# Optimization experiments

Hardware: AMD Instinct MI355X
Metric: run time of the kernel (lower is better)

The kernel has to match this reference:

```python
import jax, jax.numpy as jnp
import numpy as np

N_NODES = 8192
N_EDGES = 32768
D = 768
H1 = 8
NEG_SLOPE = 0.2


def setup_inputs() -> dict:
    key = jax.random.key(0)
    ks = jax.random.split(key, 10)
    s = 0.02  # init scale keeps attention logits numerically tame
    x = jax.random.normal(ks[0], (N_NODES, D), dtype=jnp.float32)
    edge_index = jax.random.randint(ks[1], (2, N_EDGES), 0, N_NODES, dtype=jnp.int64)
    W1 = jax.random.normal(ks[2], (D, H1 * D), dtype=jnp.float32) * s
    a_src1 = jax.random.normal(ks[3], (H1, D), dtype=jnp.float32) * s
    a_dst1 = jax.random.normal(ks[4], (H1, D), dtype=jnp.float32) * s
    b1 = jnp.zeros((H1 * D,), dtype=jnp.float32)
    W2 = jax.random.normal(ks[5], (H1 * D, D), dtype=jnp.float32) * s
    a_src2 = jax.random.normal(ks[6], (1, D), dtype=jnp.float32) * s
    a_dst2 = jax.random.normal(ks[7], (1, D), dtype=jnp.float32) * s
    b2 = jnp.zeros((D,), dtype=jnp.float32)
    return {"x": x, "edge_index": edge_index, "W1": W1, "a_src1": a_src1,
            "a_dst1": a_dst1, "b1": b1, "W2": W2, "a_src2": a_src2,
            "a_dst2": a_dst2, "b2": b2}


def gat_conv(x, src, dst, W, a_src, a_dst, b, heads, out_ch):
    """PyG GATConv (concat=True, self-loops already appended to src/dst)."""
    n = x.shape[0]
    h = (x @ W).reshape(n, heads, out_ch)            # [N,H,C]
    alpha_src = jnp.einsum("nhc,hc->nh", h, a_src)  # [N,H]
    alpha_dst = jnp.einsum("nhc,hc->nh", h, a_dst)  # [N,H]
    # edge scores: leaky_relu(a_src.h_j + a_dst.h_i) for edge j->i
    e = jax.nn.leaky_relu(alpha_src[src] + alpha_dst[dst], NEG_SLOPE)  # [E,H]
    # segment softmax over incoming edges of each destination node
    m = jax.ops.segment_max(e, dst, num_segments=n)   # [N,H]
    m = jnp.where(jnp.isfinite(m), m, 0.0)
    p = jnp.exp(e - m[dst])                           # [E,H]
    denom = jax.ops.segment_sum(p, dst, num_segments=n)
    alpha = p / denom[dst]                            # [E,H]
    msg = h[src] * alpha[:, :, None]                  # [E,H,C] gather+weight
    out = jax.ops.segment_sum(msg, dst, num_segments=n)  # [N,H,C] scatter-add
    return out.reshape(n, heads * out_ch) + b


def reference(x, edge_index, W1, a_src1, a_dst1, b1, W2, a_src2, a_dst2, b2):
    n = x.shape[0]
    loops = jnp.arange(n, dtype=edge_index.dtype)
    src = jnp.concatenate([edge_index[0], loops])  # add_self_loops=True
    dst = jnp.concatenate([edge_index[1], loops])
    h = gat_conv(x, src, dst, W1, a_src1, a_dst1, b1, H1, D)
    h = jax.nn.elu(h)
    out = gat_conv(h, src, dst, W2, a_src2, a_dst2, b2, 1, D)
    return out
```

## Files before the change

kernel.cpp:

```cpp
#include <hip/hip_runtime.h>
#include <hip/hip_bf16.h>


#define N_NODES 8192
#define N_EDGES 32768
#define E_TOT   (N_EDGES + N_NODES)
#define D_IN    768
#define H1      8
#define HC1     (H1 * D_IN)
#define KSPLIT  4
#define KSLICE  (HC1 / KSPLIT)

typedef unsigned short ushort_t;
using short8  = __attribute__((ext_vector_type(8))) short;
using floatx4 = __attribute__((ext_vector_type(4))) float;

__device__ __forceinline__ float bf2f(unsigned short u) {
  return __uint_as_float(((unsigned)u) << 16);
}
__device__ __forceinline__ unsigned short f2bf(float f) {
  unsigned u = __float_as_uint(f);
  unsigned r = (u + 0x7fffu + ((u >> 16) & 1u)) >> 16;
  return (unsigned short)r;
}

__global__ __launch_bounds__(64) void frag_transpose_kernel(
    const float* __restrict__ W, ushort_t* __restrict__ out,
    int Kdim, int Ndim) {
  const int bn = blockIdx.x;
  const int bk = blockIdx.y;
  const int lane = threadIdx.x;
  const int lrow = lane & 15, lq = lane >> 4;
  const int n = bn * 16 + lrow;
  const int kb = bk * 32 + lq * 8;
  ushort_t v[8];
#pragma unroll
  for (int e = 0; e < 8; ++e)
    v[e] = f2bf(W[(size_t)(kb + e) * Ndim + n]);
  *(short8*)(out + ((size_t)bn * (Kdim >> 5) + bk) * 512 + lane * 8) =
      *(short8*)v;
}

__global__ void prep_aw_kernel(const float* __restrict__ W1,
                               const float* __restrict__ aS,
                               const float* __restrict__ aD,
                               float* __restrict__ awS,
                               float* __restrict__ awD) {
  const int d = blockIdx.x;
  const int t = threadIdx.x;
  const float* row = W1 + (size_t)d * HC1;
  float ps[H1], pd[H1];
#pragma unroll
  for (int h = 0; h < H1; ++h) { ps[h] = 0.f; pd[h] = 0.f; }
#pragma unroll
  for (int h = 0; h < H1; ++h)
#pragma unroll
    for (int j = 0; j < 3; ++j) {
      int idx = h * 768 + j * 256 + t;
      float w = row[idx];
      ps[h] += w * aS[idx];
      pd[h] += w * aD[idx];
    }
#pragma unroll
  for (int h = 0; h < H1; ++h)
    for (int off = 32; off > 0; off >>= 1) {
      ps[h] += __shfl_down(ps[h], off, 64);
      pd[h] += __shfl_down(pd[h], off, 64);
    }
  __shared__ float red[2][4][H1];
  int w = t >> 6;
  if ((t & 63) == 0) {
#pragma unroll
    for (int h = 0; h < H1; ++h) { red[0][w][h] = ps[h]; red[1][w][h] = pd[h]; }
  }
  __syncthreads();
  if (t < H1)
    awS[d * H1 + t] = red[0][0][t] + red[0][1][t] + red[0][2][t] + red[0][3][t];
  else if (t >= 64 && t < 64 + H1) {
    int h = t - 64;
    awD[d * H1 + h] = red[1][0][h] + red[1][1][h] + red[1][2][h] + red[1][3][h];
  }
}

__global__ void node_prep_kernel(const float* __restrict__ x,
                                 const float* __restrict__ awS,
                                 const float* __restrict__ awD,
                                 ushort_t* __restrict__ xb,
                                 float* __restrict__ as1,
                                 float* __restrict__ ad1) {
  const int n = blockIdx.x;
  const int t = threadIdx.x;
  float ps[H1], pd[H1];
#pragma unroll
  for (int h = 0; h < H1; ++h) { ps[h] = 0.f; pd[h] = 0.f; }
#pragma unroll
  for (int j = 0; j < 3; ++j) {
    int d = j * 256 + t;
    float xv = x[(size_t)n * 768 + d];
    xb[(size_t)n * 768 + d] = f2bf(xv);
    const float4* s4 = (const float4*)(awS + d * 8);
    const float4* d4 = (const float4*)(awD + d * 8);
    float4 a0 = s4[0], a1 = s4[1];
    float4 c0 = d4[0], c1 = d4[1];
    ps[0] += xv * a0.x; ps[1] += xv * a0.y; ps[2] += xv * a0.z; ps[3] += xv * a0.w;
    ps[4] += xv * a1.x; ps[5] += xv * a1.y; ps[6] += xv * a1.z; ps[7] += xv * a1.w;
    pd[0] += xv * c0.x; pd[1] += xv * c0.y; pd[2] += xv * c0.z; pd[3] += xv * c0.w;
    pd[4] += xv * c1.x; pd[5] += xv * c1.y; pd[6] += xv * c1.z; pd[7] += xv * c1.w;
  }
#pragma unroll
  for (int h = 0; h < H1; ++h)
    for (int off = 32; off > 0; off >>= 1) {
      ps[h] += __shfl_down(ps[h], off, 64);
      pd[h] += __shfl_down(pd[h], off, 64);
    }
  __shared__ float red[2][4][H1];
  int w = t >> 6;
  if ((t & 63) == 0) {
#pragma unroll
    for (int h = 0; h < H1; ++h) { red[0][w][h] = ps[h]; red[1][w][h] = pd[h]; }
  }
  __syncthreads();
  if (t < H1)
    as1[n * H1 + t] = red[0][0][t] + red[0][1][t] + red[0][2][t] + red[0][3][t];
  else if (t >= 64 && t < 64 + H1) {
    int h = t - 64;
    ad1[n * H1 + h] = red[1][0][h] + red[1][1][h] + red[1][2][h] + red[1][3][h];
  }
}

__global__ void deg_kernel(const int* __restrict__ dst, int* __restrict__ deg) {
  int e = blockIdx.x * blockDim.x + threadIdx.x;
  if (e >= E_TOT) return;
  int d = (e < N_EDGES) ? dst[e] : (e - N_EDGES);
  atomicAdd(&deg[d], 1);
}

__global__ void scan_kernel(const int* __restrict__ deg, int* __restrict__ start,
                            int* __restrict__ cursor) {
  __shared__ int sums[1024];
  int t = threadIdx.x;
  int base = t * 8;
  int local[8];
  int s = 0;
#pragma unroll
  for (int i = 0; i < 8; ++i) { local[i] = s; s += deg[base + i]; }
  sums[t] = s;
  __syncthreads();
  for (int off = 1; off < 1024; off <<= 1) {
    int v = (t >= off) ? sums[t - off] : 0;
    __syncthreads();
    sums[t] += v;
    __syncthreads();
  }
  int excl = (t == 0) ? 0 : sums[t - 1];
#pragma unroll
  for (int i = 0; i < 8; ++i) {
    int st = excl + local[i];
    start[base + i] = st;
    cursor[base + i] = st;
  }
}

__global__ void fill_kernel(const int* __restrict__ dst, int* __restrict__ cursor,
                            int* __restrict__ csr) {
  int e = blockIdx.x * blockDim.x + threadIdx.x;
  if (e >= E_TOT) return;
  int d = (e < N_EDGES) ? dst[e] : (e - N_EDGES);
  int pos = atomicAdd(&cursor[d], 1);
  csr[pos] = e;
}

__global__ __launch_bounds__(256) void attn1_kernel(
    const ushort_t* __restrict__ xb, const float* __restrict__ as1,
    const float* __restrict__ ad1, const int* __restrict__ start,
    const int* __restrict__ deg, const int* __restrict__ csr,
    const int* __restrict__ src, ushort_t* __restrict__ z_sw) {
  const int n = blockIdx.x;
  const int t = threadIdx.x;
  const int st = start[n], dg = deg[n];
  const int h = t & 7, eloc = t >> 3;
  __shared__ float invd[H1];
  __shared__ float alphaS[32][H1];
  __shared__ int sidx[32];
  __shared__ float red[4][H1];

  const float adv = ad1[n * H1 + h];
  float pden = 0.f;
  for (int base = 0; base < dg; base += 32) {
    int ei = base + eloc;
    if (ei < dg) {
      int e = csr[st + ei];
      int s = (e < N_EDGES) ? src[e] : (e - N_EDGES);
      float l = as1[s * H1 + h] + adv;
      l = l > 0.f ? l : 0.2f * l;
      pden += __expf(l);
    }
  }
  pden += __shfl_down(pden, 8, 64);
  pden += __shfl_down(pden, 16, 64);
  pden += __shfl_down(pden, 32, 64);
  if ((t & 63) < 8) red[t >> 6][h] = pden;
  __syncthreads();
  if (t < 8) invd[t] = 1.0f / (red[0][t] + red[1][t] + red[2][t] + red[3][t]);
  __syncthreads();

  int hp[3], ip[3];
#pragma unroll
  for (int p = 0; p < 3; ++p) {
    int c8 = p * 256 + t;
    hp[p] = c8 / 96;
    ip[p] = c8 % 96;
  }
  float acc[3][8];
#pragma unroll
  for (int p = 0; p < 3; ++p)
#pragma unroll
    for (int e = 0; e < 8; ++e) acc[p][e] = 0.f;

  for (int base = 0; base < dg; base += 32) {
    int cnt = dg - base; if (cnt > 32) cnt = 32;
    if (eloc < cnt) {
      int e = csr[st + base + eloc];
      int s = (e < N_EDGES) ? src[e] : (e - N_EDGES);
      float l = as1[s * H1 + h] + adv;
      l = l > 0.f ? l : 0.2f * l;
      alphaS[eloc][h] = __expf(l) * invd[h];
      if (h == 0) sidx[eloc] = s;
    }
    __syncthreads();
    for (int ei = 0; ei < cnt; ++ei) {
      int s = sidx[ei];
      const uint4* xrow = (const uint4*)(xb + (size_t)s * 768);
#pragma unroll
      for (int p = 0; p < 3; ++p) {
        uint4 v = xrow[ip[p]];
        float al = alphaS[ei][hp[p]];
        unsigned uu[4] = {v.x, v.y, v.z, v.w};
#pragma unroll
        for (int q = 0; q < 4; ++q) {
          acc[p][2 * q]     += al * __uint_as_float(uu[q] << 16);
          acc[p][2 * q + 1] += al * __uint_as_float(uu[q] & 0xffff0000u);
        }
      }
    }
    __syncthreads();
  }
#pragma unroll
  for (int p = 0; p < 3; ++p) {
    int c8 = p * 256 + t;
    int k = c8 * 8;
    size_t chunk = (size_t)(n >> 4) * 192 + (k >> 5);
    int word = ((k >> 3) & 3) * 16 + (n & 15);
    ushort_t v[8];
#pragma unroll
    for (int e = 0; e < 8; ++e) v[e] = f2bf(acc[p][e]);
    *(short8*)(z_sw + chunk * 512 + word * 8) = *(short8*)v;
  }
}

#define LOADI(dst, BASE, CH, kk)                                               \
  _Pragma("unroll") for (int q = 0; q < 4; ++q)                                \
      dst[q] = *(const short8*)((BASE) +                                       \
                                (((size_t)((CH)[q] + (kk))) << 9) + lane8);

#define MFMA16(af, bf)                                                         \
  _Pragma("unroll") for (int i_ = 0; i_ < 4; ++i_)                             \
      _Pragma("unroll") for (int j_ = 0; j_ < 4; ++j_)                         \
          acc[i_][j_] = __builtin_amdgcn_mfma_f32_16x16x32_bf16(               \
              af[i_], bf[j_], acc[i_][j_], 0, 0, 0);

#define GEMM_KLOOP(NCH, ABASE, BBASE)                                          \
  {                                                                            \
    short8 a0[4], b0[4], a1[4], b1[4];                                         \
    LOADI(a0, ABASE, chA, 0) LOADI(b0, BBASE, chB, 0)                          \
    LOADI(a1, ABASE, chA, 1) LOADI(b1, BBASE, chB, 1)                          \
    for (int k = 0; k < (NCH); k += 2) {                                       \
      MFMA16(a0, b0)                                                           \
      LOADI(a0, ABASE, chA, k + 2) LOADI(b0, BBASE, chB, k + 2)                \
      MFMA16(a1, b1)                                                           \
      LOADI(a1, ABASE, chA, k + 3) LOADI(b1, BBASE, chB, k + 3)                \
    }                                                                          \
  }

__global__ __launch_bounds__(256) void gemm_l1_kernel(
    const ushort_t* __restrict__ Asw, const ushort_t* __restrict__ Bsw,
    const float* __restrict__ biasb, ushort_t* __restrict__ Csw) {
  __shared__ ushort_t tile[128 * 136];
  const int id = blockIdx.x;
  const int head = id & 7;
  const int j_id = id >> 3;
  const int n_t = j_id % 6;
  const int m_t = j_id / 6;
  const int tid = threadIdx.x;
  const int lane = tid & 63;
  const int w = tid >> 6;
  const int wm = w >> 1, wn = w & 1;
  const int lrow = lane & 15, lq = lane >> 4;
  const int lane8 = lane * 8;

  int chA[4], chB[4];
#pragma unroll
  for (int q = 0; q < 4; ++q) {
    chA[q] = __builtin_amdgcn_readfirstlane((m_t * 8 + wm * 4 + q) * 192 +
                                            head * 24);
    chB[q] = __builtin_amdgcn_readfirstlane((head * 48 + n_t * 8 + wn * 4 + q) *
                                            24);
  }
  floatx4 acc[4][4];
#pragma unroll
  for (int i = 0; i < 4; ++i)
#pragma unroll
    for (int j = 0; j < 4; ++j) acc[i][j] = {0.f, 0.f, 0.f, 0.f};

  GEMM_KLOOP(24, Asw, Bsw)

  const float* bias = biasb + head * 768 + n_t * 128;
#pragma unroll
  for (int i = 0; i < 4; ++i) {
    int row_l = wm * 64 + i * 16 + lq * 4;
#pragma unroll
    for (int j = 0; j < 4; ++j) {
      int col_l = wn * 64 + j * 16 + lrow;
      float bv = bias[col_l];
#pragma unroll
      for (int r = 0; r < 4; ++r) {
        float v = acc[i][j][r] + bv;
        v = v > 0.f ? v : __expf(v) - 1.0f;
        tile[(row_l + r) * 136 + col_l] = f2bf(v);
      }
    }
  }
  __syncthreads();
#pragma unroll
  for (int cc = 0; cc < 8; ++cc) {
    int ch = w * 8 + cc;
    int RB = ch >> 2, kg = ch & 3;
    short8 vv = *(const short8*)&tile[(RB * 16 + lrow) * 136 + kg * 32 + lq * 8];
    size_t chunk_g = (size_t)(m_t * 8 + RB) * 192 + head * 24 + n_t * 4 + kg;
    *((short8*)Csw + chunk_g * 64 + lane) = vv;
  }
}

__global__ __launch_bounds__(256) void gemm_l2_kernel(
    const ushort_t* __restrict__ Asw, const ushort_t* __restrict__ Bsw,
    float* __restrict__ Cp) {
  const int id = blockIdx.x;
  const int c = id & 7;
  const int s = c >> 1;
  const int j_id = id >> 3;
  const int n_t = j_id % 6;
  const int m_t = (j_id / 6) * 2 + (c & 1);
  const int tid = threadIdx.x;
  const int lane = tid & 63;
  const int w = tid >> 6;
  const int wm = w >> 1, wn = w & 1;
  const int lrow = lane & 15, lq = lane >> 4;
  const int lane8 = lane * 8;

  int chA[4], chB[4];
#pragma unroll
  for (int q = 0; q < 4; ++q) {
    chA[q] = __builtin_amdgcn_readfirstlane((m_t * 8 + wm * 4 + q) * 192 +
                                            s * 48);
    chB[q] = __builtin_amdgcn_readfirstlane((n_t * 8 + wn * 4 + q) * 192 +
                                            s * 48);
  }
  floatx4 acc[4][4];
#pragma unroll
  for (int i = 0; i < 4; ++i)
#pragma unroll
    for (int j = 0; j < 4; ++j) acc[i][j] = {0.f, 0.f, 0.f, 0.f};

  GEMM_KLOOP(48, Asw, Bsw)

  float* C = Cp + (size_t)s * N_NODES * 768;
  const int m0 = m_t * 128, n0 = n_t * 128;
#pragma unroll
  for (int i = 0; i < 4; ++i) {
    int row_b = m0 + wm * 64 + i * 16 + lq * 4;
#pragma unroll
    for (int j = 0; j < 4; ++j) {
      int col = n0 + wn * 64 + j * 16 + lrow;
#pragma unroll
      for (int r = 0; r < 4; ++r)
        C[(size_t)(row_b + r) * 768 + col] = acc[i][j][r];
    }
  }
}

__global__ void reduce_alpha2_kernel(const float* __restrict__ parts,
                                     const float* __restrict__ aS,
                                     const float* __restrict__ aD,
                                     ushort_t* __restrict__ yb,
                                     float* __restrict__ as2,
                                     float* __restrict__ ad2) {
  const int n = blockIdx.x;
  const int t = threadIdx.x;
  const size_t S = (size_t)N_NODES * 768;
  float ps = 0.f, pd = 0.f;
#pragma unroll
  for (int j = 0; j < 3; ++j) {
    int cidx = j * 256 + t;
    size_t base = (size_t)n * 768 + cidx;
    float v = parts[base] + parts[base + S] + parts[base + 2 * S] +
              parts[base + 3 * S];
    yb[base] = f2bf(v);
    ps += v * aS[cidx];
    pd += v * aD[cidx];
  }
  for (int off = 32; off > 0; off >>= 1) {
    ps += __shfl_down(ps, off, 64);
    pd += __shfl_down(pd, off, 64);
  }
  __shared__ float red[2][4];
  int w = t >> 6;
  if ((t & 63) == 0) { red[0][w] = ps; red[1][w] = pd; }
  __syncthreads();
  if (t == 0) as2[n] = red[0][0] + red[0][1] + red[0][2] + red[0][3];
  if (t == 64) ad2[n] = red[1][0] + red[1][1] + red[1][2] + red[1][3];
}

__global__ __launch_bounds__(256) void attn2_kernel(
    const ushort_t* __restrict__ yb, const float* __restrict__ as2,
    const float* __restrict__ ad2, const int* __restrict__ start,
    const int* __restrict__ deg, const int* __restrict__ csr,
    const int* __restrict__ src, const float* __restrict__ b2,
    float* __restrict__ out) {
  const int n = blockIdx.x;
  const int t = threadIdx.x;
  const int st = start[n], dg = deg[n];
  __shared__ float alphaS[64];
  __shared__ int sidx[64];
  __shared__ float red[4];
  __shared__ float invd_sh;

  const float adv = ad2[n];
  float pden = 0.f;
  for (int ei = t; ei < dg; ei += 256) {
    int e = csr[st + ei];
    int s = (e < N_EDGES) ? src[e] : (e - N_EDGES);
    float l = as2[s] + adv;
    l = l > 0.f ? l : 0.2f * l;
    pden += __expf(l);
  }
  for (int off = 32; off > 0; off >>= 1) pden += __shfl_down(pden, off, 64);
  if ((t & 63) == 0) red[t >> 6] = pden;
  __syncthreads();
  if (t == 0) invd_sh = 1.0f / (red[0] + red[1] + red[2] + red[3]);
  __syncthreads();
  const float invd = invd_sh;

  float a0 = 0.f, a1 = 0.f, a2 = 0.f;
  for (int base = 0; base < dg; base += 64) {
    int cnt = dg - base; if (cnt > 64) cnt = 64;
    if (t < cnt) {
      int e = csr[st + base + t];
      int s = (e < N_EDGES) ? src[e] : (e - N_EDGES);
      float l = as2[s] + adv;
      l = l > 0.f ? l : 0.2f * l;
      alphaS[t] = __expf(l) * invd;
      sidx[t] = s;
    }
    __syncthreads();
    for (int ei = 0; ei < cnt; ++ei) {
      float al = alphaS[ei];
      const ushort_t* row = yb + (size_t)sidx[ei] * 768;
      a0 += al * bf2f(row[t]);
      a1 += al * bf2f(row[t + 256]);
      a2 += al * bf2f(row[t + 512]);
    }
    __syncthreads();
  }
  out[(size_t)n * 768 + t]       = a0 + b2[t];
  out[(size_t)n * 768 + t + 256] = a1 + b2[t + 256];
  out[(size_t)n * 768 + t + 512] = a2 + b2[t + 512];
}

extern "C" void kernel_launch(void* const* d_in, const int* in_sizes, int n_in,
                              void* d_out, int out_size, void* d_ws, size_t ws_size,
                              hipStream_t stream) {
  const float* x      = (const float*)d_in[0];
  const int*   ei     = (const int*)d_in[1];
  const float* W1     = (const float*)d_in[2];
  const float* a_src1 = (const float*)d_in[3];
  const float* a_dst1 = (const float*)d_in[4];
  const float* b1     = (const float*)d_in[5];
  const float* W2     = (const float*)d_in[6];
  const float* a_src2 = (const float*)d_in[7];
  const float* a_dst2 = (const float*)d_in[8];
  const float* b2     = (const float*)d_in[9];
  float* out = (float*)d_out;
  const int* src = ei;
  const int* dst = ei + N_EDGES;

  char* ws = (char*)d_ws;
  size_t off = 0;
  auto alloc = [&](size_t bytes) -> void* {
    void* p = ws + off;
    off = (off + bytes + 255) & ~(size_t)255;
    return p;
  };

  int* deg = (int*)alloc(N_NODES * 4);
  float* awS = (float*)alloc(768 * H1 * 4);
  float* awD = (float*)alloc(768 * H1 * 4);
  float* as1 = (float*)alloc(N_NODES * H1 * 4);
  float* ad1 = (float*)alloc(N_NODES * H1 * 4);
  float* as2 = (float*)alloc(N_NODES * 4);
  float* ad2 = (float*)alloc(N_NODES * 4);
  int* start  = (int*)alloc(N_NODES * 4);
  int* cursor = (int*)alloc(N_NODES * 4);
  int* csr    = (int*)alloc(E_TOT * 4);
  ushort_t* xb     = (ushort_t*)alloc((size_t)N_NODES * D_IN * 2);
  ushort_t* w1t_sw = (ushort_t*)alloc((size_t)HC1 * D_IN * 2 + 8192);
  ushort_t* w2t_sw = (ushort_t*)alloc((size_t)HC1 * D_IN * 2 + 8192);
  ushort_t* z_sw   = (ushort_t*)alloc((size_t)N_NODES * HC1 * 2 + 8192);
  ushort_t* h2b_sw = (ushort_t*)alloc((size_t)N_NODES * HC1 * 2 + 8192);
  ushort_t* yb  = xb;
  float* parts  = (float*)z_sw;
  (void)ws_size; (void)n_in; (void)in_sizes; (void)out_size;

  hipMemsetAsync(deg, 0, N_NODES * 4, stream);

  prep_aw_kernel<<<768, 256, 0, stream>>>(W1, a_src1, a_dst1, awS, awD);
  node_prep_kernel<<<N_NODES, 256, 0, stream>>>(x, awS, awD, xb, as1, ad1);
  frag_transpose_kernel<<<dim3(HC1 / 16, D_IN / 32), 64, 0, stream>>>(
      W1, w1t_sw, D_IN, HC1);
  frag_transpose_kernel<<<dim3(D_IN / 16, HC1 / 32), 64, 0, stream>>>(
      W2, w2t_sw, HC1, D_IN);

  deg_kernel<<<(E_TOT + 255) / 256, 256, 0, stream>>>(dst, deg);
  scan_kernel<<<1, 1024, 0, stream>>>(deg, start, cursor);
  fill_kernel<<<(E_TOT + 255) / 256, 256, 0, stream>>>(dst, cursor, csr);

  attn1_kernel<<<N_NODES, 256, 0, stream>>>(xb, as1, ad1, start, deg, csr,
                                            src, z_sw);
  gemm_l1_kernel<<<8 * 64 * 6, 256, 0, stream>>>(z_sw, w1t_sw, b1, h2b_sw);

  gemm_l2_kernel<<<KSPLIT * 2 * 32 * 6, 256, 0, stream>>>(h2b_sw, w2t_sw,
                                                          parts);
  reduce_alpha2_kernel<<<N_NODES, 256, 0, stream>>>(parts, a_src2, a_dst2, yb,
                                                    as2, ad2);
  attn2_kernel<<<N_NODES, 256, 0, stream>>>(yb, as2, ad2, start, deg, csr,
                                            src, b2, out);
}
```

Measured before the change: 511.6 us.

## Stage GEMM operand fragments through LDS with double-buffered global_load_lds

New measurement: 490.4 us. 1.04x faster.

```diff
diff --git a/kernel.cpp b/kernel.cpp
--- a/kernel.cpp
+++ b/kernel.cpp
@@ -22,6 +22,12 @@
   unsigned u = __float_as_uint(f);
   unsigned r = (u + 0x7fffu + ((u >> 16) & 1u)) >> 16;
   return (unsigned short)r;
+}
+
+__device__ __forceinline__ void gll16(const ushort_t* g, ushort_t* l) {
+  __builtin_amdgcn_global_load_lds(
+      (const __attribute__((address_space(1))) void*)g,
+      (__attribute__((address_space(3))) void*)l, 16, 0, 0);
 }
 
 __global__ __launch_bounds__(64) void frag_transpose_kernel(
@@ -258,34 +264,47 @@
   }
 }
 
-#define LOADI(dst, BASE, CH, kk)                                               \
-  _Pragma("unroll") for (int q = 0; q < 4; ++q)                                \
-      dst[q] = *(const short8*)((BASE) +                                       \
-                                (((size_t)((CH)[q] + (kk))) << 9) + lane8);
-
 #define MFMA16(af, bf)                                                         \
   _Pragma("unroll") for (int i_ = 0; i_ < 4; ++i_)                             \
       _Pragma("unroll") for (int j_ = 0; j_ < 4; ++j_)                         \
           acc[i_][j_] = __builtin_amdgcn_mfma_f32_16x16x32_bf16(               \
               af[i_], bf[j_], acc[i_][j_], 0, 0, 0);
 
-#define GEMM_KLOOP(NCH, ABASE, BBASE)                                          \
+#define STAGE16(b, kc)                                                         \
   {                                                                            \
-    short8 a0[4], b0[4], a1[4], b1[4];                                         \
-    LOADI(a0, ABASE, chA, 0) LOADI(b0, BBASE, chB, 0)                          \
-    LOADI(a1, ABASE, chA, 1) LOADI(b1, BBASE, chB, 1)                          \
-    for (int k = 0; k < (NCH); k += 2) {                                       \
-      MFMA16(a0, b0)                                                           \
-      LOADI(a0, ABASE, chA, k + 2) LOADI(b0, BBASE, chB, k + 2)                \
-      MFMA16(a1, b1)                                                           \
-      LOADI(a1, ABASE, chA, k + 3) LOADI(b1, BBASE, chB, k + 3)                \
+    ushort_t* ld_ = smem + (b) * 8192 + (2 * w) * 512;                         \
+    gll16(ASW + (((size_t)(cA0 + (kc))) << 9) + lane8, ld_);                   \
+    gll16(ASW + (((size_t)(cA1 + (kc))) << 9) + lane8, ld_ + 512);             \
+    gll16(BSW + (((size_t)(cB0 + (kc))) << 9) + lane8, ld_ + 4096);            \
+    gll16(BSW + (((size_t)(cB1 + (kc))) << 9) + lane8, ld_ + 4608);            \
+  }
+
+#define SBODY(b, kc, NCH)                                                      \
+  {                                                                            \
+    if ((kc) + 1 < (NCH)) STAGE16((b) ^ 1, (kc) + 1)                           \
+    const ushort_t* ra_ = smem + (b) * 8192 + wm * 2048 + lane8;               \
+    const ushort_t* rb_ = smem + (b) * 8192 + 4096 + wn * 2048 + lane8;        \
+    short8 af[4], bf[4];                                                       \
+    _Pragma("unroll") for (int q_ = 0; q_ < 4; ++q_) {                         \
+      af[q_] = *(const short8*)(ra_ + q_ * 512);                               \
+      bf[q_] = *(const short8*)(rb_ + q_ * 512);                               \
     }                                                                          \
+    MFMA16(af, bf)                                                             \
+    __syncthreads();                                                           \
+  }
+
+#define STAGED_KLOOP(NCH)                                                      \
+  STAGE16(0, 0)                                                                \
+  __syncthreads();                                                             \
+  for (int kc = 0; kc < (NCH); kc += 2) {                                      \
+    SBODY(0, kc, (NCH))                                                        \
+    SBODY(1, kc + 1, (NCH))                                                    \
   }
 
 __global__ __launch_bounds__(256) void gemm_l1_kernel(
     const ushort_t* __restrict__ Asw, const ushort_t* __restrict__ Bsw,
     const float* __restrict__ biasb, ushort_t* __restrict__ Csw) {
-  __shared__ ushort_t tile[128 * 136];
+  __shared__ ushort_t smem[17408];
   const int id = blockIdx.x;
   const int head = id & 7;
   const int j_id = id >> 3;
@@ -297,23 +316,25 @@
   const int wm = w >> 1, wn = w & 1;
   const int lrow = lane & 15, lq = lane >> 4;
   const int lane8 = lane * 8;
-
-  int chA[4], chB[4];
-#pragma unroll
-  for (int q = 0; q < 4; ++q) {
-    chA[q] = __builtin_amdgcn_readfirstlane((m_t * 8 + wm * 4 + q) * 192 +
-                                            head * 24);
-    chB[q] = __builtin_amdgcn_readfirstlane((head * 48 + n_t * 8 + wn * 4 + q) *
-                                            24);
-  }
+  const ushort_t* ASW = Asw;
+  const ushort_t* BSW = Bsw;
+
+  const int cA0 = __builtin_amdgcn_readfirstlane((m_t * 8 + 2 * w) * 192 +
+                                                 head * 24);
+  const int cA1 = cA0 + 192;
+  const int cB0 = __builtin_amdgcn_readfirstlane((head * 48 + n_t * 8 + 2 * w) *
+                                                 24);
+  const int cB1 = cB0 + 24;
+
   floatx4 acc[4][4];
 #pragma unroll
   for (int i = 0; i < 4; ++i)
 #pragma unroll
     for (int j = 0; j < 4; ++j) acc[i][j] = {0.f, 0.f, 0.f, 0.f};
 
-  GEMM_KLOOP(24, Asw, Bsw)
-
+  STAGED_KLOOP(24)
+
+  ushort_t* tile = smem;
   const float* bias = biasb + head * 768 + n_t * 128;
 #pragma unroll
   for (int i = 0; i < 4; ++i) {
@@ -344,6 +365,7 @@
 __global__ __launch_bounds__(256) void gemm_l2_kernel(
     const ushort_t* __restrict__ Asw, const ushort_t* __restrict__ Bsw,
     float* __restrict__ Cp) {
+  __shared__ ushort_t smem[16384];
   const int id = blockIdx.x;
   const int c = id & 7;
   const int s = c >> 1;
@@ -356,22 +378,23 @@
   const int wm = w >> 1, wn = w & 1;
   const int lrow = lane & 15, lq = lane >> 4;
   const int lane8 = lane * 8;
-
-  int chA[4], chB[4];
-#pragma unroll
-  for (int q = 0; q < 4; ++q) {
-    chA[q] = __builtin_amdgcn_readfirstlane((m_t * 8 + wm * 4 + q) * 192 +
-                                            s * 48);
-    chB[q] = __builtin_amdgcn_readfirstlane((n_t * 8 + wn * 4 + q) * 192 +
-                                            s * 48);
-  }
+  const ushort_t* ASW = Asw;
+  const ushort_t* BSW = Bsw;
+
+  const int cA0 = __builtin_amdgcn_readfirstlane((m_t * 8 + 2 * w) * 192 +
+                                                 s * 48);
+  const int cA1 = cA0 + 192;
+  const int cB0 = __builtin_amdgcn_readfirstlane((n_t * 8 + 2 * w) * 192 +
+                                                 s * 48);
+  const int cB1 = cB0 + 192;
+
   floatx4 acc[4][4];
 #pragma unroll
   for (int i = 0; i < 4; ++i)
 #pragma unroll
     for (int j = 0; j < 4; ++j) acc[i][j] = {0.f, 0.f, 0.f, 0.f};
 
-  GEMM_KLOOP(48, Asw, Bsw)
+  STAGED_KLOOP(48)
 
   float* C = Cp + (size_t)s * N_NODES * 768;
   const int m0 = m_t * 128, n0 = n_t * 128;
```

## Stage GEMM operands through LDS ring with async global_load_lds and larger tiles

Applied to the files above, without the earlier changes.

After: 462.4 us. 9.6% less time.

```diff
diff --git a/kernel.cpp b/kernel.cpp
--- a/kernel.cpp
+++ b/kernel.cpp
@@ -22,6 +22,12 @@
   unsigned u = __float_as_uint(f);
   unsigned r = (u + 0x7fffu + ((u >> 16) & 1u)) >> 16;
   return (unsigned short)r;
+}
+
+__device__ __forceinline__ void gll16(const ushort_t* g, ushort_t* l) {
+  __builtin_amdgcn_global_load_lds(
+      (const __attribute__((address_space(1))) void*)g,
+      (__attribute__((address_space(3))) void*)l, 16, 0, 0);
 }
 
 __global__ __launch_bounds__(64) void frag_transpose_kernel(
@@ -258,126 +264,154 @@
   }
 }
 
-#define LOADI(dst, BASE, CH, kk)                                               \
-  _Pragma("unroll") for (int q = 0; q < 4; ++q)                                \
-      dst[q] = *(const short8*)((BASE) +                                       \
-                                (((size_t)((CH)[q] + (kk))) << 9) + lane8);
-
-#define MFMA16(af, bf)                                                         \
-  _Pragma("unroll") for (int i_ = 0; i_ < 4; ++i_)                             \
-      _Pragma("unroll") for (int j_ = 0; j_ < 4; ++j_)                         \
-          acc[i_][j_] = __builtin_amdgcn_mfma_f32_16x16x32_bf16(               \
-              af[i_], bf[j_], acc[i_][j_], 0, 0, 0);
-
-#define GEMM_KLOOP(NCH, ABASE, BBASE)                                          \
+#define STAGE_RING(t)                                                          \
   {                                                                            \
-    short8 a0[4], b0[4], a1[4], b1[4];                                         \
-    LOADI(a0, ABASE, chA, 0) LOADI(b0, BBASE, chB, 0)                          \
-    LOADI(a1, ABASE, chA, 1) LOADI(b1, BBASE, chB, 1)                          \
-    for (int k = 0; k < (NCH); k += 2) {                                       \
-      MFMA16(a0, b0)                                                           \
-      LOADI(a0, ABASE, chA, k + 2) LOADI(b0, BBASE, chB, k + 2)                \
-      MFMA16(a1, b1)                                                           \
-      LOADI(a1, ABASE, chA, k + 3) LOADI(b1, BBASE, chB, k + 3)                \
-    }                                                                          \
-  }
-
-__global__ __launch_bounds__(256) void gemm_l1_kernel(
+    ushort_t* ld_ = smem + ((t) & 3) * 16384 + slot512;                        \
+    _Pragma("unroll") for (int q_ = 0; q_ < 4; ++q_)                           \
+        gll16(SRC + (((size_t)(cb[q_] + (t))) << 9) + lane8, ld_ + q_ * 512);  \
+  }
+
+#define GSTEP_BODY(s, VMSTR, NSV)                                             \
+  {                                                                           \
+    asm volatile("s_waitcnt vmcnt(" VMSTR ")" ::: "memory");                  \
+    __builtin_amdgcn_s_barrier();                                             \
+    if ((s) + 3 < (NSV)) STAGE_RING((s) + 3)                                  \
+    const ushort_t* buf_ = smem + ((s) & 3) * 16384;                          \
+    short8 af[8], bf[4];                                                      \
+    _Pragma("unroll") for (int i_ = 0; i_ < 8; ++i_)                          \
+        af[i_] = *(const short8*)(buf_ + (wm * 8 + i_) * 512 + lane8);        \
+    _Pragma("unroll") for (int j_ = 0; j_ < 4; ++j_)                          \
+        bf[j_] = *(const short8*)(buf_ + 8192 + (wn * 4 + j_) * 512 + lane8); \
+    __builtin_amdgcn_s_setprio(1);                                            \
+    _Pragma("unroll") for (int i_ = 0; i_ < 8; ++i_)                          \
+        _Pragma("unroll") for (int j_ = 0; j_ < 4; ++j_)                      \
+            acc[i_][j_] = __builtin_amdgcn_mfma_f32_16x16x32_bf16(            \
+                af[i_], bf[j_], acc[i_][j_], 0, 0, 0);                        \
+    __builtin_amdgcn_s_setprio(0);                                            \
+  }
+
+#define GEMM_PIPE(NSV)                                                        \
+  _Pragma("unroll") for (int p_ = 0; p_ < 3; ++p_) STAGE_RING(p_)             \
+  _Pragma("unroll 4") for (int s_ = 0; s_ < (NSV)-2; ++s_) {                  \
+    GSTEP_BODY(s_, "8", (NSV))                                                \
+  }                                                                           \
+  GSTEP_BODY((NSV)-2, "4", (NSV))                                             \
+  GSTEP_BODY((NSV)-1, "0", (NSV))
+
+__global__ __launch_bounds__(512, 2) void gemm_l1_kernel(
     const ushort_t* __restrict__ Asw, const ushort_t* __restrict__ Bsw,
     const float* __restrict__ biasb, ushort_t* __restrict__ Csw) {
-  __shared__ ushort_t tile[128 * 136];
+  __shared__ ushort_t smem[4 * 16384];
   const int id = blockIdx.x;
   const int head = id & 7;
   const int j_id = id >> 3;
-  const int n_t = j_id % 6;
-  const int m_t = j_id / 6;
+  const int n_t = j_id % 3;
+  const int m_t = j_id / 3;
   const int tid = threadIdx.x;
   const int lane = tid & 63;
   const int w = tid >> 6;
-  const int wm = w >> 1, wn = w & 1;
+  const int wm = w >> 2, wn = w & 3;
   const int lrow = lane & 15, lq = lane >> 4;
   const int lane8 = lane * 8;
-
-  int chA[4], chB[4];
+  const int slot512 = w * 2048;
+  const ushort_t* SRC = (w < 4) ? Asw : Bsw;
+
+  int cb[4];
 #pragma unroll
   for (int q = 0; q < 4; ++q) {
-    chA[q] = __builtin_amdgcn_readfirstlane((m_t * 8 + wm * 4 + q) * 192 +
-                                            head * 24);
-    chB[q] = __builtin_amdgcn_readfirstlane((head * 48 + n_t * 8 + wn * 4 + q) *
-                                            24);
-  }
-  floatx4 acc[4][4];
-#pragma unroll
-  for (int i = 0; i < 4; ++i)
+    int v;
+    if (w < 4)
+      v = (m_t * 16 + 4 * w + q) * 192 + head * 24;
+    else
+      v = (head * 48 + n_t * 16 + 4 * (w - 4) + q) * 24;
+    cb[q] = __builtin_amdgcn_readfirstlane(v);
+  }
+
+  floatx4 acc[8][4];
+#pragma unroll
+  for (int i = 0; i < 8; ++i)
 #pragma unroll
     for (int j = 0; j < 4; ++j) acc[i][j] = {0.f, 0.f, 0.f, 0.f};
 
-  GEMM_KLOOP(24, Asw, Bsw)
-
-  const float* bias = biasb + head * 768 + n_t * 128;
-#pragma unroll
-  for (int i = 0; i < 4; ++i) {
-    int row_l = wm * 64 + i * 16 + lq * 4;
-#pragma unroll
-    for (int j = 0; j < 4; ++j) {
-      int col_l = wn * 64 + j * 16 + lrow;
-      float bv = bias[col_l];
-#pragma unroll
-      for (int r = 0; r < 4; ++r) {
-        float v = acc[i][j][r] + bv;
-        v = v > 0.f ? v : __expf(v) - 1.0f;
-        tile[(row_l + r) * 136 + col_l] = f2bf(v);
-      }
-    }
-  }
-  __syncthreads();
-#pragma unroll
-  for (int cc = 0; cc < 8; ++cc) {
-    int ch = w * 8 + cc;
-    int RB = ch >> 2, kg = ch & 3;
-    short8 vv = *(const short8*)&tile[(RB * 16 + lrow) * 136 + kg * 32 + lq * 8];
-    size_t chunk_g = (size_t)(m_t * 8 + RB) * 192 + head * 24 + n_t * 4 + kg;
-    *((short8*)Csw + chunk_g * 64 + lane) = vv;
-  }
-}
-
-__global__ __launch_bounds__(256) void gemm_l2_kernel(
+  GEMM_PIPE(24)
+
+  ushort_t* tile = smem;
+  const float* bias = biasb + head * 768 + n_t * 256;
+#pragma unroll
+  for (int p = 0; p < 2; ++p) {
+    if (p) __syncthreads();
+    if (wm == p) {
+#pragma unroll
+      for (int i = 0; i < 8; ++i)
+#pragma unroll
+        for (int j = 0; j < 4; ++j) {
+          int col = wn * 64 + j * 16 + lrow;
+          float bv = bias[col];
+#pragma unroll
+          for (int r = 0; r < 4; ++r) {
+            float v = acc[i][j][r] + bv;
+            v = v > 0.f ? v : __expf(v) - 1.0f;
+            tile[(i * 16 + lq * 4 + r) * 280 + col] = f2bf(v);
+          }
+        }
+    }
+    __syncthreads();
+#pragma unroll
+    for (int cc = 0; cc < 8; ++cc) {
+      int ch = w * 8 + cc;
+      int RB = ch >> 3, kg = ch & 7;
+      short8 vv =
+          *(const short8*)&tile[(RB * 16 + lrow) * 280 + kg * 32 + lq * 8];
+      size_t chunk_g = (size_t)(m_t * 16 + p * 8 + RB) * 192 + head * 24 +
+                       n_t * 8 + kg;
+      *((short8*)Csw + chunk_g * 64 + lane) = vv;
+    }
+  }
+}
+
+__global__ __launch_bounds__(512, 2) void gemm_l2_kernel(
     const ushort_t* __restrict__ Asw, const ushort_t* __restrict__ Bsw,
     float* __restrict__ Cp) {
+  __shared__ ushort_t smem[4 * 16384];
   const int id = blockIdx.x;
   const int c = id & 7;
-  const int s = c >> 1;
+  const int sl = c >> 1;
   const int j_id = id >> 3;
-  const int n_t = j_id % 6;
-  const int m_t = (j_id / 6) * 2 + (c & 1);
+  const int n_t = j_id % 3;
+  const int m_t = (j_id / 3) * 2 + (c & 1);
   const int tid = threadIdx.x;
   const int lane = tid & 63;
   const int w = tid >> 6;
-  const int wm = w >> 1, wn = w & 1;
+  const int wm = w >> 2, wn = w & 3;
   const int lrow = lane & 15, lq = lane >> 4;
   const int lane8 = lane * 8;
-
-  int chA[4], chB[4];
+  const int slot512 = w * 2048;
+  const ushort_t* SRC = (w < 4) ? Asw : Bsw;
+
+  int cb[4];
 #pragma unroll
   for (int q = 0; q < 4; ++q) {
-    chA[q] = __builtin_amdgcn_readfirstlane((m_t * 8 + wm * 4 + q) * 192 +
-                                            s * 48);
-    chB[q] = __builtin_amdgcn_readfirstlane((n_t * 8 + wn * 4 + q) * 192 +
-                                            s * 48);
-  }
-  floatx4 acc[4][4];
-#pragma unroll
-  for (int i = 0; i < 4; ++i)
+    int v;
+    if (w < 4)
+      v = (m_t * 16 + 4 * w + q) * 192 + sl * 48;
+    else
+      v = (n_t * 16 + 4 * (w - 4) + q) * 192 + sl * 48;
+    cb[q] = __builtin_amdgcn_readfirstlane(v);
+  }
+
+  floatx4 acc[8][4];
+#pragma unroll
+  for (int i = 0; i < 8; ++i)
 #pragma unroll
     for (int j = 0; j < 4; ++j) acc[i][j] = {0.f, 0.f, 0.f, 0.f};
 
-  GEMM_KLOOP(48, Asw, Bsw)
-
-  float* C = Cp + (size_t)s * N_NODES * 768;
-  const int m0 = m_t * 128, n0 = n_t * 128;
-#pragma unroll
-  for (int i = 0; i < 4; ++i) {
-    int row_b = m0 + wm * 64 + i * 16 + lq * 4;
+  GEMM_PIPE(48)
+
+  float* C = Cp + (size_t)sl * N_NODES * 768;
+  const int m0 = m_t * 256, n0 = n_t * 256;
+#pragma unroll
+  for (int i = 0; i < 8; ++i) {
+    int row_b = m0 + wm * 128 + i * 16 + lq * 4;
 #pragma unroll
     for (int j = 0; j < 4; ++j) {
       int col = n0 + wn * 64 + j * 16 + lrow;
@@ -535,9 +569,9 @@
 
   attn1_kernel<<<N_NODES, 256, 0, stream>>>(xb, as1, ad1, start, deg, csr,
                                             src, z_sw);
-  gemm_l1_kernel<<<8 * 64 * 6, 256, 0, stream>>>(z_sw, w1t_sw, b1, h2b_sw);
-
-  gemm_l2_kernel<<<KSPLIT * 2 * 32 * 6, 256, 0, stream>>>(h2b_sw, w2t_sw,
+  gemm_l1_kernel<<<8 * 32 * 3, 512, 0, stream>>>(z_sw, w1t_sw, b1, h2b_sw);
+
+  gemm_l2_kernel<<<KSPLIT * 2 * 16 * 3, 512, 0, stream>>>(h2b_sw, w2t_sw,
                                                           parts);
   reduce_alpha2_kernel<<<N_NODES, 256, 0, stream>>>(parts, a_src2, a_dst2, yb,
                                                     as2, ad2);
```
